# Performance work log

Hardware: AMD Instinct MI355X
Metric: run time of the kernel (lower is better)

The kernel has to match this reference:

```python
import jax, jax.numpy as jnp
import numpy as np

EPS = 1e-8

def _cdist(a, b):
    # Euclidean pairwise distances, torch.cdist(p=2) equivalent.
    sq = (jnp.sum(a * a, axis=1)[:, None] + jnp.sum(b * b, axis=1)[None, :]
          - 2.0 * (a @ b.T))
    return jnp.sqrt(jnp.maximum(sq, 1e-12))

def setup_inputs() -> dict:
    key = jax.random.key(0)
    k1, k2, k3, k4, k5, k6 = jax.random.split(key, 6)
    ns, n_cls, n_feat, K = 4096, 500, 256, 400
    return {
        "src_x": jax.random.normal(k1, (ns, n_feat), dtype=jnp.float32),
        "tgt_x": jax.random.normal(k2, (ns, n_feat), dtype=jnp.float32),
        "src_y": jax.random.uniform(k3, (ns, n_cls), dtype=jnp.float32),
        "tgt_y": jax.random.uniform(k4, (ns, n_cls), dtype=jnp.float32),
        "queue": jax.random.normal(k5, (n_cls, n_feat, K), dtype=jnp.float32),
        "queue_size": jax.random.randint(k6, (n_cls,), 0, K, dtype=jnp.int32),
    }

def reference(src_x, tgt_x, src_y, tgt_y, queue, queue_size):
    n_cls, n_feat, K = queue.shape
    num = queue_size.astype(queue.dtype)[:, None]                      # (C,1)
    # src_centroid: masked mean over the first queue_size[c] columns
    valid = (jnp.arange(K)[None, :] < queue_size[:, None]).astype(queue.dtype)  # (C,K)
    centroid = jnp.einsum('cfk,ck->cf', queue, valid) / jnp.maximum(num, 1.0)
    centroid = jnp.where(num > 0, centroid, 0.0)                       # (C,F)

    batch_src = src_y.T @ src_x                                        # (C,F)
    total_num = num + jnp.sum(src_y, axis=0)[:, None] + EPS            # (C,1)
    mean_src = (centroid * num + batch_src) / total_num                # (C,F)

    batch_prob = jnp.sum(tgt_y, axis=0)[:, None] + EPS                 # (C,1)
    mean_tgt = (tgt_y.T @ tgt_x) / batch_prob                          # (C,F)

    intra = jnp.diagonal(_cdist(mean_src, mean_tgt)).mean()
    inter = _cdist(mean_src, mean_src).mean()
    return intra, inter
```

## Files before the change

### kernel.cpp

```cpp
#include <hip/hip_runtime.h>
#include <math.h>

#define NS 4096
#define NC 500
#define NF 256
#define NK 400
#define KC_GEMM 8
#define NB_GEMM (KC_GEMM * 32 * 2)
#define NQB 4000

__global__ __launch_bounds__(256) void k_heavy(
    const float* __restrict__ Xs, const float* __restrict__ Ys, float* __restrict__ Ps,
    const float* __restrict__ Xt, const float* __restrict__ Yt, float* __restrict__ Pt,
    float* __restrict__ CSs, float* __restrict__ CSt,
    const float* __restrict__ queue, const int* __restrict__ qsize,
    float* __restrict__ qsum) {
  __shared__ float ytile[256][16];
  __shared__ float csbuf[256];
  const int bid  = blockIdx.x;
  const int tid  = threadIdx.x;
  const int w    = tid >> 6;
  const int lane = tid & 63;

  if (bid < NB_GEMM) {
    const int z   = bid >> 8;
    const int rem = bid & 255;
    const int kc  = rem >> 5;
    const int c0  = (rem & 31) * 16;
    const float* X = z ? Xt : Xs;
    const float* Y = z ? Yt : Ys;
    float*       P = z ? Pt : Ps;
    float*      CS = z ? CSt : CSs;
    const int n0   = kc * 512;
    const int cmax = (NC - c0 < 16) ? (NC - c0) : 16;

    float acc[16];
    #pragma unroll
    for (int j = 0; j < 16; ++j) acc[j] = 0.f;
    float csum = 0.f;

    for (int p = 0; p < 2; ++p) {
      {
        const int rr = tid >> 4, cc = tid & 15;
        #pragma unroll
        for (int j = 0; j < 16; ++j) {
          float v = (cc < cmax)
              ? Y[(size_t)(n0 + p * 256 + rr + 16 * j) * NC + c0 + cc] : 0.f;
          ytile[rr + 16 * j][cc] = v;
          csum += v;
        }
      }
      __syncthreads();

      const float* Xp = X + (size_t)(n0 + p * 256) * NF + tid;
      #pragma unroll 4
      for (int n = 0; n < 256; ++n) {
        float xv = Xp[(size_t)n * NF];
        float4 y0 = *reinterpret_cast<const float4*>(&ytile[n][0]);
        float4 y1 = *reinterpret_cast<const float4*>(&ytile[n][4]);
        float4 y2 = *reinterpret_cast<const float4*>(&ytile[n][8]);
        float4 y3 = *reinterpret_cast<const float4*>(&ytile[n][12]);
        acc[0]  = fmaf(y0.x, xv, acc[0]);  acc[1]  = fmaf(y0.y, xv, acc[1]);
        acc[2]  = fmaf(y0.z, xv, acc[2]);  acc[3]  = fmaf(y0.w, xv, acc[3]);
        acc[4]  = fmaf(y1.x, xv, acc[4]);  acc[5]  = fmaf(y1.y, xv, acc[5]);
        acc[6]  = fmaf(y1.z, xv, acc[6]);  acc[7]  = fmaf(y1.w, xv, acc[7]);
        acc[8]  = fmaf(y2.x, xv, acc[8]);  acc[9]  = fmaf(y2.y, xv, acc[9]);
        acc[10] = fmaf(y2.z, xv, acc[10]); acc[11] = fmaf(y2.w, xv, acc[11]);
        acc[12] = fmaf(y3.x, xv, acc[12]); acc[13] = fmaf(y3.y, xv, acc[13]);
        acc[14] = fmaf(y3.z, xv, acc[14]); acc[15] = fmaf(y3.w, xv, acc[15]);
      }
      __syncthreads();
    }

    csbuf[tid] = csum;
    __syncthreads();
    if (tid < 16) {
      float t = 0.f;
      #pragma unroll
      for (int j = 0; j < 16; ++j) t += csbuf[tid + 16 * j];
      CS[kc * 512 + c0 + tid] = t;
    }

    #pragma unroll
    for (int j = 0; j < 16; ++j)
      if (j < cmax) P[((size_t)kc * NC + c0 + j) * NF + tid] = acc[j];

  } else {
    const int qb = bid - NB_GEMM;
    const int r0 = (qb * 4 + w) * 8;
    const int c  = r0 >> 8;
    const int qs = qsize[c];
    const int L  = (qs + 3) >> 2;
    const float* base = queue + (size_t)r0 * NK;
    float s0 = 0.f, s1 = 0.f, s2 = 0.f, s3 = 0.f;
    float s4 = 0.f, s5 = 0.f, s6 = 0.f, s7 = 0.f;

    if (lane < L) {
      const int k = 4 * lane;
      float4 v0 = *reinterpret_cast<const float4*>(base + 0 * NK + k);
      float4 v1 = *reinterpret_cast<const float4*>(base + 1 * NK + k);
      float4 v2 = *reinterpret_cast<const float4*>(base + 2 * NK + k);
      float4 v3 = *reinterpret_cast<const float4*>(base + 3 * NK + k);
      float4 v4 = *reinterpret_cast<const float4*>(base + 4 * NK + k);
      float4 v5 = *reinterpret_cast<const float4*>(base + 5 * NK + k);
      float4 v6 = *reinterpret_cast<const float4*>(base + 6 * NK + k);
      float4 v7 = *reinterpret_cast<const float4*>(base + 7 * NK + k);
      s0 += v0.x; s1 += v1.x; s2 += v2.x; s3 += v3.x;
      s4 += v4.x; s5 += v5.x; s6 += v6.x; s7 += v7.x;
      if (k + 1 < qs) { s0 += v0.y; s1 += v1.y; s2 += v2.y; s3 += v3.y;
                        s4 += v4.y; s5 += v5.y; s6 += v6.y; s7 += v7.y; }
      if (k + 2 < qs) { s0 += v0.z; s1 += v1.z; s2 += v2.z; s3 += v3.z;
                        s4 += v4.z; s5 += v5.z; s6 += v6.z; s7 += v7.z; }
      if (k + 3 < qs) { s0 += v0.w; s1 += v1.w; s2 += v2.w; s3 += v3.w;
                        s4 += v4.w; s5 += v5.w; s6 += v6.w; s7 += v7.w; }
    }
    if (lane + 64 < L) {
      const int k = 256 + 4 * lane;
      float4 v0 = *reinterpret_cast<const float4*>(base + 0 * NK + k);
      float4 v1 = *reinterpret_cast<const float4*>(base + 1 * NK + k);
      float4 v2 = *reinterpret_cast<const float4*>(base + 2 * NK + k);
      float4 v3 = *reinterpret_cast<const float4*>(base + 3 * NK + k);
      float4 v4 = *reinterpret_cast<const float4*>(base + 4 * NK + k);
      float4 v5 = *reinterpret_cast<const float4*>(base + 5 * NK + k);
      float4 v6 = *reinterpret_cast<const float4*>(base + 6 * NK + k);
      float4 v7 = *reinterpret_cast<const float4*>(base + 7 * NK + k);
      s0 += v0.x; s1 += v1.x; s2 += v2.x; s3 += v3.x;
      s4 += v4.x; s5 += v5.x; s6 += v6.x; s7 += v7.x;
      if (k + 1 < qs) { s0 += v0.y; s1 += v1.y; s2 += v2.y; s3 += v3.y;
                        s4 += v4.y; s5 += v5.y; s6 += v6.y; s7 += v7.y; }
      if (k + 2 < qs) { s0 += v0.z; s1 += v1.z; s2 += v2.z; s3 += v3.z;
                        s4 += v4.z; s5 += v5.z; s6 += v6.z; s7 += v7.z; }
      if (k + 3 < qs) { s0 += v0.w; s1 += v1.w; s2 += v2.w; s3 += v3.w;
                        s4 += v4.w; s5 += v5.w; s6 += v6.w; s7 += v7.w; }
    }
    #pragma unroll
    for (int m = 32; m; m >>= 1) {
      s0 += __shfl_xor(s0, m); s1 += __shfl_xor(s1, m);
      s2 += __shfl_xor(s2, m); s3 += __shfl_xor(s3, m);
      s4 += __shfl_xor(s4, m); s5 += __shfl_xor(s5, m);
      s6 += __shfl_xor(s6, m); s7 += __shfl_xor(s7, m);
    }
    if (lane == 0) {
      *reinterpret_cast<float4*>(&qsum[r0])     = make_float4(s0, s1, s2, s3);
      *reinterpret_cast<float4*>(&qsum[r0 + 4]) = make_float4(s4, s5, s6, s7);
    }
  }
}

__global__ __launch_bounds__(256) void k_means(
    const float* __restrict__ qsum, const int* __restrict__ qsize,
    const float* __restrict__ Psrc, const float* __restrict__ Ptgt,
    const float* __restrict__ CSsrc, const float* __restrict__ CStgt,
    float* __restrict__ MS, float* __restrict__ MT, float* __restrict__ ipart) {
  const int c = blockIdx.x;
  const int f = threadIdx.x;

  float cs_s = 0.f, cs_t = 0.f;
  #pragma unroll
  for (int kc = 0; kc < KC_GEMM; ++kc) {
    cs_s += CSsrc[kc * 512 + c];
    cs_t += CStgt[kc * 512 + c];
  }
  float num = (float)qsize[c];
  float ns = qsum[(size_t)c * NF + f];
  float nt = 0.f;
  #pragma unroll
  for (int kc = 0; kc < KC_GEMM; ++kc) {
    ns += Psrc[((size_t)kc * NC + c) * NF + f];
    nt += Ptgt[((size_t)kc * NC + c) * NF + f];
  }
  float ms = ns / (num + cs_s + 1e-8f);
  float mt = nt / (cs_t + 1e-8f);
  MS[(size_t)c * NF + f] = ms;
  MT[(size_t)c * NF + f] = mt;

  float d = ms - mt;
  float s = d * d;
  #pragma unroll
  for (int m = 32; m; m >>= 1) s += __shfl_xor(s, m);
  __shared__ float red[4];
  int wid = f >> 6, lane = f & 63;
  if (lane == 0) red[wid] = s;
  __syncthreads();
  if (f == 0) ipart[c] = sqrtf(fmaxf(red[0] + red[1] + red[2] + red[3], 1e-12f));
}

#define TC 16
#define NBT 32
__global__ __launch_bounds__(256) void k_dist(const float* __restrict__ MS,
                                              float* __restrict__ epart) {
  __shared__ float a[TC][NF + 4];
  __shared__ float b[TC][NF + 4];
  const int bi = blockIdx.x & (NBT - 1);
  const int bj = blockIdx.x >> 5;

  for (int i = threadIdx.x; i < TC * (NF / 4); i += 256) {
    int rr = i >> 6, fq = (i & 63) * 4;
    int c1 = bi * TC + rr;
    int c2 = bj * TC + rr;
    float4 va = (c1 < NC) ? *reinterpret_cast<const float4*>(&MS[(size_t)c1 * NF + fq])
                          : make_float4(0.f, 0.f, 0.f, 0.f);
    float4 vb = (c2 < NC) ? *reinterpret_cast<const float4*>(&MS[(size_t)c2 * NF + fq])
                          : make_float4(0.f, 0.f, 0.f, 0.f);
    *reinterpret_cast<float4*>(&a[rr][fq]) = va;
    *reinterpret_cast<float4*>(&b[rr][fq]) = vb;
  }
  __syncthreads();

  const int i1 = threadIdx.x >> 4, i2 = threadIdx.x & 15;
  float s = 0.f;
  #pragma unroll 8
  for (int fq = 0; fq < NF; fq += 4) {
    float4 va = *reinterpret_cast<const float4*>(&a[i1][fq]);
    float4 vb = *reinterpret_cast<const float4*>(&b[i2][fq]);
    float d0 = va.x - vb.x, d1 = va.y - vb.y, d2 = va.z - vb.z, d3 = va.w - vb.w;
    s = fmaf(d0, d0, s); s = fmaf(d1, d1, s); s = fmaf(d2, d2, s); s = fmaf(d3, d3, s);
  }
  bool valid = (bi * TC + i1 < NC) && (bj * TC + i2 < NC);
  float rr = valid ? sqrtf(fmaxf(s, 1e-12f)) : 0.f;

  #pragma unroll
  for (int m = 32; m; m >>= 1) rr += __shfl_xor(rr, m);
  __shared__ float red[4];
  int wid = threadIdx.x >> 6, lane = threadIdx.x & 63;
  if (lane == 0) red[wid] = rr;
  __syncthreads();
  if (threadIdx.x == 0) epart[blockIdx.x] = red[0] + red[1] + red[2] + red[3];
}

__global__ __launch_bounds__(1024) void k_final(const float* __restrict__ ipart,
                                                const float* __restrict__ epart,
                                                float* __restrict__ out) {
  const int t = threadIdx.x;
  float si = (t < NC) ? ipart[t] : 0.f;
  float se = epart[t];
  #pragma unroll
  for (int m = 32; m; m >>= 1) { si += __shfl_xor(si, m); se += __shfl_xor(se, m); }
  __shared__ float ri[16], re[16];
  int wid = t >> 6, lane = t & 63;
  if (lane == 0) { ri[wid] = si; re[wid] = se; }
  __syncthreads();
  if (t == 0) {
    float A = 0.f, B = 0.f;
    #pragma unroll
    for (int w2 = 0; w2 < 16; ++w2) { A += ri[w2]; B += re[w2]; }
    out[0] = A / (float)NC;
    out[1] = B / ((float)NC * (float)NC);
  }
}

extern "C" void kernel_launch(void* const* d_in, const int* in_sizes, int n_in,
                              void* d_out, int out_size, void* d_ws, size_t ws_size,
                              hipStream_t stream) {
  const float* src_x = (const float*)d_in[0];
  const float* tgt_x = (const float*)d_in[1];
  const float* src_y = (const float*)d_in[2];
  const float* tgt_y = (const float*)d_in[3];
  const float* queue = (const float*)d_in[4];
  const int*   qsize = (const int*)d_in[5];
  float* out = (float*)d_out;

  float* ws    = (float*)d_ws;
  float* qsum  = ws;
  float* Psrc  = qsum + NC * NF;
  float* Ptgt  = Psrc + (size_t)KC_GEMM * NC * NF;
  float* CSs   = Ptgt + (size_t)KC_GEMM * NC * NF;
  float* CSt   = CSs + KC_GEMM * 512;
  float* MS    = CSt + KC_GEMM * 512;
  float* MT    = MS + NC * NF;
  float* ipart = MT + NC * NF;
  float* epart = ipart + NC;

  k_heavy<<<NB_GEMM + NQB, 256, 0, stream>>>(
      src_x, src_y, Psrc, tgt_x, tgt_y, Ptgt, CSs, CSt, queue, qsize, qsum);

  k_means<<<NC, 256, 0, stream>>>(qsum, qsize, Psrc, Ptgt, CSs, CSt, MS, MT, ipart);

  k_dist<<<NBT * NBT, 256, 0, stream>>>(MS, epart);

  k_final<<<1, 1024, 0, stream>>>(ipart, epart, out);
}
```

Before: 82.85 us.

## Co-schedule GEMM and queue-reduction warps in the same blocks with finer K-split

Launches 1024 blocks of 512 threads instead of separate GEMM and queue blocks. In each block, four warps compute a 256-row GEMM chunk (the K split doubles to 16) while the other four warps each do four queue-sum jobs. The aim is to overlap the compute-bound partial GEMM with the bandwidth-bound masked queue reduction on every CU. The cost is twice as many partial-product slices to write and later reduce in k_means. Larger blocks may also limit occupancy.

```diff
diff --git a/kernel.cpp b/kernel.cpp
--- a/kernel.cpp
+++ b/kernel.cpp
@@ -5,11 +5,10 @@
 #define NC 500
 #define NF 256
 #define NK 400
-#define KC_GEMM 8
-#define NB_GEMM (KC_GEMM * 32 * 2)
-#define NQB 4000
-
-__global__ __launch_bounds__(256) void k_heavy(
+#define KC_GEMM 16
+#define NQWJ 16000
+
+__global__ __launch_bounds__(512) void k_heavy(
     const float* __restrict__ Xs, const float* __restrict__ Ys, float* __restrict__ Ps,
     const float* __restrict__ Xt, const float* __restrict__ Yt, float* __restrict__ Pt,
     float* __restrict__ CSs, float* __restrict__ CSt,
@@ -22,58 +21,50 @@
   const int w    = tid >> 6;
   const int lane = tid & 63;
 
-  if (bid < NB_GEMM) {
-    const int z   = bid >> 8;
-    const int rem = bid & 255;
-    const int kc  = rem >> 5;
-    const int c0  = (rem & 31) * 16;
+  const int z  = bid >> 9;
+  const int kc = (bid >> 5) & 15;
+  const int c0 = (bid & 31) * 16;
+
+  if (w < 4) {
     const float* X = z ? Xt : Xs;
     const float* Y = z ? Yt : Ys;
     float*       P = z ? Pt : Ps;
     float*      CS = z ? CSt : CSs;
-    const int n0   = kc * 512;
+    const int n0   = kc * 256;
     const int cmax = (NC - c0 < 16) ? (NC - c0) : 16;
 
+    float csum = 0.f;
+    for (int i = tid; i < 256 * 16; i += 256) {
+      int rr = i >> 4, cc = i & 15;
+      float v = (cc < cmax) ? Y[(size_t)(n0 + rr) * NC + c0 + cc] : 0.f;
+      ytile[rr][cc] = v;
+      csum += v;
+    }
+    csbuf[tid] = csum;
+    __syncthreads();
+
+    const int f = tid;
     float acc[16];
     #pragma unroll
     for (int j = 0; j < 16; ++j) acc[j] = 0.f;
-    float csum = 0.f;
-
-    for (int p = 0; p < 2; ++p) {
-      {
-        const int rr = tid >> 4, cc = tid & 15;
-        #pragma unroll
-        for (int j = 0; j < 16; ++j) {
-          float v = (cc < cmax)
-              ? Y[(size_t)(n0 + p * 256 + rr + 16 * j) * NC + c0 + cc] : 0.f;
-          ytile[rr + 16 * j][cc] = v;
-          csum += v;
-        }
-      }
-      __syncthreads();
-
-      const float* Xp = X + (size_t)(n0 + p * 256) * NF + tid;
-      #pragma unroll 4
-      for (int n = 0; n < 256; ++n) {
-        float xv = Xp[(size_t)n * NF];
-        float4 y0 = *reinterpret_cast<const float4*>(&ytile[n][0]);
-        float4 y1 = *reinterpret_cast<const float4*>(&ytile[n][4]);
-        float4 y2 = *reinterpret_cast<const float4*>(&ytile[n][8]);
-        float4 y3 = *reinterpret_cast<const float4*>(&ytile[n][12]);
-        acc[0]  = fmaf(y0.x, xv, acc[0]);  acc[1]  = fmaf(y0.y, xv, acc[1]);
-        acc[2]  = fmaf(y0.z, xv, acc[2]);  acc[3]  = fmaf(y0.w, xv, acc[3]);
-        acc[4]  = fmaf(y1.x, xv, acc[4]);  acc[5]  = fmaf(y1.y, xv, acc[5]);
-        acc[6]  = fmaf(y1.z, xv, acc[6]);  acc[7]  = fmaf(y1.w, xv, acc[7]);
-        acc[8]  = fmaf(y2.x, xv, acc[8]);  acc[9]  = fmaf(y2.y, xv, acc[9]);
-        acc[10] = fmaf(y2.z, xv, acc[10]); acc[11] = fmaf(y2.w, xv, acc[11]);
-        acc[12] = fmaf(y3.x, xv, acc[12]); acc[13] = fmaf(y3.y, xv, acc[13]);
-        acc[14] = fmaf(y3.z, xv, acc[14]); acc[15] = fmaf(y3.w, xv, acc[15]);
-      }
-      __syncthreads();
-    }
-
-    csbuf[tid] = csum;
-    __syncthreads();
+
+    #pragma unroll 4
+    for (int n = 0; n < 256; ++n) {
+      float xv = X[(size_t)(n0 + n) * NF + f];
+      float4 y0 = *reinterpret_cast<const float4*>(&ytile[n][0]);
+      float4 y1 = *reinterpret_cast<const float4*>(&ytile[n][4]);
+      float4 y2 = *reinterpret_cast<const float4*>(&ytile[n][8]);
+      float4 y3 = *reinterpret_cast<const float4*>(&ytile[n][12]);
+      acc[0]  = fmaf(y0.x, xv, acc[0]);  acc[1]  = fmaf(y0.y, xv, acc[1]);
+      acc[2]  = fmaf(y0.z, xv, acc[2]);  acc[3]  = fmaf(y0.w, xv, acc[3]);
+      acc[4]  = fmaf(y1.x, xv, acc[4]);  acc[5]  = fmaf(y1.y, xv, acc[5]);
+      acc[6]  = fmaf(y1.z, xv, acc[6]);  acc[7]  = fmaf(y1.w, xv, acc[7]);
+      acc[8]  = fmaf(y2.x, xv, acc[8]);  acc[9]  = fmaf(y2.y, xv, acc[9]);
+      acc[10] = fmaf(y2.z, xv, acc[10]); acc[11] = fmaf(y2.w, xv, acc[11]);
+      acc[12] = fmaf(y3.x, xv, acc[12]); acc[13] = fmaf(y3.y, xv, acc[13]);
+      acc[14] = fmaf(y3.z, xv, acc[14]); acc[15] = fmaf(y3.w, xv, acc[15]);
+    }
+
     if (tid < 16) {
       float t = 0.f;
       #pragma unroll
@@ -83,66 +74,72 @@
 
     #pragma unroll
     for (int j = 0; j < 16; ++j)
-      if (j < cmax) P[((size_t)kc * NC + c0 + j) * NF + tid] = acc[j];
+      if (c0 + j < NC) P[((size_t)kc * NC + c0 + j) * NF + f] = acc[j];
 
   } else {
-    const int qb = bid - NB_GEMM;
-    const int r0 = (qb * 4 + w) * 8;
-    const int c  = r0 >> 8;
-    const int qs = qsize[c];
-    const int L  = (qs + 3) >> 2;
-    const float* base = queue + (size_t)r0 * NK;
-    float s0 = 0.f, s1 = 0.f, s2 = 0.f, s3 = 0.f;
-    float s4 = 0.f, s5 = 0.f, s6 = 0.f, s7 = 0.f;
-
-    if (lane < L) {
-      const int k = 4 * lane;
-      float4 v0 = *reinterpret_cast<const float4*>(base + 0 * NK + k);
-      float4 v1 = *reinterpret_cast<const float4*>(base + 1 * NK + k);
-      float4 v2 = *reinterpret_cast<const float4*>(base + 2 * NK + k);
-      float4 v3 = *reinterpret_cast<const float4*>(base + 3 * NK + k);
-      float4 v4 = *reinterpret_cast<const float4*>(base + 4 * NK + k);
-      float4 v5 = *reinterpret_cast<const float4*>(base + 5 * NK + k);
-      float4 v6 = *reinterpret_cast<const float4*>(base + 6 * NK + k);
-      float4 v7 = *reinterpret_cast<const float4*>(base + 7 * NK + k);
-      s0 += v0.x; s1 += v1.x; s2 += v2.x; s3 += v3.x;
-      s4 += v4.x; s5 += v5.x; s6 += v6.x; s7 += v7.x;
-      if (k + 1 < qs) { s0 += v0.y; s1 += v1.y; s2 += v2.y; s3 += v3.y;
-                        s4 += v4.y; s5 += v5.y; s6 += v6.y; s7 += v7.y; }
-      if (k + 2 < qs) { s0 += v0.z; s1 += v1.z; s2 += v2.z; s3 += v3.z;
-                        s4 += v4.z; s5 += v5.z; s6 += v6.z; s7 += v7.z; }
-      if (k + 3 < qs) { s0 += v0.w; s1 += v1.w; s2 += v2.w; s3 += v3.w;
-                        s4 += v4.w; s5 += v5.w; s6 += v6.w; s7 += v7.w; }
-    }
-    if (lane + 64 < L) {
-      const int k = 256 + 4 * lane;
-      float4 v0 = *reinterpret_cast<const float4*>(base + 0 * NK + k);
-      float4 v1 = *reinterpret_cast<const float4*>(base + 1 * NK + k);
-      float4 v2 = *reinterpret_cast<const float4*>(base + 2 * NK + k);
-      float4 v3 = *reinterpret_cast<const float4*>(base + 3 * NK + k);
-      float4 v4 = *reinterpret_cast<const float4*>(base + 4 * NK + k);
-      float4 v5 = *reinterpret_cast<const float4*>(base + 5 * NK + k);
-      float4 v6 = *reinterpret_cast<const float4*>(base + 6 * NK + k);
-      float4 v7 = *reinterpret_cast<const float4*>(base + 7 * NK + k);
-      s0 += v0.x; s1 += v1.x; s2 += v2.x; s3 += v3.x;
-      s4 += v4.x; s5 += v5.x; s6 += v6.x; s7 += v7.x;
-      if (k + 1 < qs) { s0 += v0.y; s1 += v1.y; s2 += v2.y; s3 += v3.y;
-                        s4 += v4.y; s5 += v5.y; s6 += v6.y; s7 += v7.y; }
-      if (k + 2 < qs) { s0 += v0.z; s1 += v1.z; s2 += v2.z; s3 += v3.z;
-                        s4 += v4.z; s5 += v5.z; s6 += v6.z; s7 += v7.z; }
-      if (k + 3 < qs) { s0 += v0.w; s1 += v1.w; s2 += v2.w; s3 += v3.w;
-                        s4 += v4.w; s5 += v5.w; s6 += v6.w; s7 += v7.w; }
-    }
-    #pragma unroll
-    for (int m = 32; m; m >>= 1) {
-      s0 += __shfl_xor(s0, m); s1 += __shfl_xor(s1, m);
-      s2 += __shfl_xor(s2, m); s3 += __shfl_xor(s3, m);
-      s4 += __shfl_xor(s4, m); s5 += __shfl_xor(s5, m);
-      s6 += __shfl_xor(s6, m); s7 += __shfl_xor(s7, m);
-    }
-    if (lane == 0) {
-      *reinterpret_cast<float4*>(&qsum[r0])     = make_float4(s0, s1, s2, s3);
-      *reinterpret_cast<float4*>(&qsum[r0 + 4]) = make_float4(s4, s5, s6, s7);
+    __syncthreads();
+
+    const int qw = w - 4;
+    for (int jj = 0; jj < 4; ++jj) {
+      const int q = bid * 16 + qw * 4 + jj;
+      if (q >= NQWJ) break;
+      const int r0 = q * 8;
+      const int c  = r0 >> 8;
+      const int qs = qsize[c];
+      const int L  = (qs + 3) >> 2;
+      const float* base = queue + (size_t)r0 * NK;
+      float s0 = 0.f, s1 = 0.f, s2 = 0.f, s3 = 0.f;
+      float s4 = 0.f, s5 = 0.f, s6 = 0.f, s7 = 0.f;
+
+      if (lane < L) {
+        const int k = 4 * lane;
+        float4 v0 = *reinterpret_cast<const float4*>(base + 0 * NK + k);
+        float4 v1 = *reinterpret_cast<const float4*>(base + 1 * NK + k);
+        float4 v2 = *reinterpret_cast<const float4*>(base + 2 * NK + k);
+        float4 v3 = *reinterpret_cast<const float4*>(base + 3 * NK + k);
+        float4 v4 = *reinterpret_cast<const float4*>(base + 4 * NK + k);
+        float4 v5 = *reinterpret_cast<const float4*>(base + 5 * NK + k);
+        float4 v6 = *reinterpret_cast<const float4*>(base + 6 * NK + k);
+        float4 v7 = *reinterpret_cast<const float4*>(base + 7 * NK + k);
+        s0 += v0.x; s1 += v1.x; s2 += v2.x; s3 += v3.x;
+        s4 += v4.x; s5 += v5.x; s6 += v6.x; s7 += v7.x;
+        if (k + 1 < qs) { s0 += v0.y; s1 += v1.y; s2 += v2.y; s3 += v3.y;
+                          s4 += v4.y; s5 += v5.y; s6 += v6.y; s7 += v7.y; }
+        if (k + 2 < qs) { s0 += v0.z; s1 += v1.z; s2 += v2.z; s3 += v3.z;
+                          s4 += v4.z; s5 += v5.z; s6 += v6.z; s7 += v7.z; }
+        if (k + 3 < qs) { s0 += v0.w; s1 += v1.w; s2 += v2.w; s3 += v3.w;
+                          s4 += v4.w; s5 += v5.w; s6 += v6.w; s7 += v7.w; }
+      }
+      if (lane + 64 < L) {
+        const int k = 256 + 4 * lane;
+        float4 v0 = *reinterpret_cast<const float4*>(base + 0 * NK + k);
+        float4 v1 = *reinterpret_cast<const float4*>(base + 1 * NK + k);
+        float4 v2 = *reinterpret_cast<const float4*>(base + 2 * NK + k);
+        float4 v3 = *reinterpret_cast<const float4*>(base + 3 * NK + k);
+        float4 v4 = *reinterpret_cast<const float4*>(base + 4 * NK + k);
+        float4 v5 = *reinterpret_cast<const float4*>(base + 5 * NK + k);
+        float4 v6 = *reinterpret_cast<const float4*>(base + 6 * NK + k);
+        float4 v7 = *reinterpret_cast<const float4*>(base + 7 * NK + k);
+        s0 += v0.x; s1 += v1.x; s2 += v2.x; s3 += v3.x;
+        s4 += v4.x; s5 += v5.x; s6 += v6.x; s7 += v7.x;
+        if (k + 1 < qs) { s0 += v0.y; s1 += v1.y; s2 += v2.y; s3 += v3.y;
+                          s4 += v4.y; s5 += v5.y; s6 += v6.y; s7 += v7.y; }
+        if (k + 2 < qs) { s0 += v0.z; s1 += v1.z; s2 += v2.z; s3 += v3.z;
+                          s4 += v4.z; s5 += v5.z; s6 += v6.z; s7 += v7.z; }
+        if (k + 3 < qs) { s0 += v0.w; s1 += v1.w; s2 += v2.w; s3 += v3.w;
+                          s4 += v4.w; s5 += v5.w; s6 += v6.w; s7 += v7.w; }
+      }
+      #pragma unroll
+      for (int m = 32; m; m >>= 1) {
+        s0 += __shfl_xor(s0, m); s1 += __shfl_xor(s1, m);
+        s2 += __shfl_xor(s2, m); s3 += __shfl_xor(s3, m);
+        s4 += __shfl_xor(s4, m); s5 += __shfl_xor(s5, m);
+        s6 += __shfl_xor(s6, m); s7 += __shfl_xor(s7, m);
+      }
+      if (lane == 0) {
+        *reinterpret_cast<float4*>(&qsum[r0])     = make_float4(s0, s1, s2, s3);
+        *reinterpret_cast<float4*>(&qsum[r0 + 4]) = make_float4(s4, s5, s6, s7);
+      }
     }
   }
 }
@@ -271,7 +268,7 @@
   float* ipart = MT + NC * NF;
   float* epart = ipart + NC;
 
-  k_heavy<<<NB_GEMM + NQB, 256, 0, stream>>>(
+  k_heavy<<<1024, 512, 0, stream>>>(
       src_x, src_y, Psrc, tgt_x, tgt_y, Ptgt, CSs, CSt, queue, qsize, qsum);
 
   k_means<<<NC, 256, 0, stream>>>(qsum, qsize, Psrc, Ptgt, CSs, CSt, MS, MT, ipart);
```

Result: slower. 90.44 us (+9.2%).
